# Kernel optimization log

Hardware: AMD Instinct MI355X
Metric: run time of the kernel (lower is better)

## Reference

```python
import jax, jax.numpy as jnp
import numpy as np

HIDDEN = 2048
N_LAYERS = 2
CHOICE_NUM = 19  # (task_num-1)*2 + 1 with task_num=10, adapt=False
VOCAB = CHOICE_NUM + 1


def setup_inputs() -> dict:
    key = jax.random.key(0)
    ks = jax.random.split(key, 16)
    s = 0.02
    inp = {}
    inp["input_idx"] = jax.random.randint(ks[0], (1,), 0, VOCAB)
    inp["task"] = 5  # python int; 1+task <= CHOICE_NUM
    inp["embedding"] = jax.random.normal(ks[1], (VOCAB, HIDDEN), dtype=jnp.float32) * s
    k = 2
    for i in range(N_LAYERS):
        inp[f"w_ih_{i}"] = jax.random.normal(ks[k + 0], (4 * HIDDEN, HIDDEN), dtype=jnp.float32) * s
        inp[f"w_hh_{i}"] = jax.random.normal(ks[k + 1], (4 * HIDDEN, HIDDEN), dtype=jnp.float32) * s
        inp[f"b_ih_{i}"] = jax.random.normal(ks[k + 2], (4 * HIDDEN,), dtype=jnp.float32) * s
        inp[f"b_hh_{i}"] = jax.random.normal(ks[k + 3], (4 * HIDDEN,), dtype=jnp.float32) * s
        k += 4
    inp["w_choice"] = jax.random.normal(ks[k], (CHOICE_NUM, HIDDEN), dtype=jnp.float32) * s
    inp["b_choice"] = jax.random.normal(ks[k + 1], (CHOICE_NUM,), dtype=jnp.float32) * s
    return inp


def _lstm_cell(x, h, c, w_ih, w_hh, b_ih, b_hh):
    # x, h, c: [1, H]; torch LSTMCell gate order: i, f, g, o
    gates = x @ w_ih.T + b_ih + h @ w_hh.T + b_hh  # [1, 4H]
    i, f, g, o = jnp.split(gates, 4, axis=-1)
    c_next = jax.nn.sigmoid(f) * c + jax.nn.sigmoid(i) * jnp.tanh(g)
    h_next = jax.nn.sigmoid(o) * jnp.tanh(c_next)
    return h_next, c_next


def reference(input_idx, task, embedding,
              w_ih_0, w_hh_0, b_ih_0, b_hh_0,
              w_ih_1, w_hh_1, b_ih_1, b_hh_1,
              w_choice, b_choice):
    x = embedding[input_idx].reshape(1, -1)  # [1, H]
    layers = [(w_ih_0, w_hh_0, b_ih_0, b_hh_0),
              (w_ih_1, w_hh_1, b_ih_1, b_hh_1)]
    zeros = jnp.zeros((1, HIDDEN), dtype=x.dtype)
    for (w_ih, w_hh, b_ih, b_hh) in layers:
        # hidden=None in the torch module -> per-layer zero initial state
        h, c = _lstm_cell(x, zeros, zeros, w_ih, w_hh, b_ih, b_hh)
        x = h
    logit = (x @ w_choice.T + b_choice).reshape(-1)  # [CHOICE_NUM]
    mask = jnp.arange(CHOICE_NUM) < (1 + task)  # adapt=False: prefix 1+task ones
    logit = jnp.where(mask, logit, jnp.float32(-1e9))
    return logit
```

## Files before the change

kernel.cpp:

```cpp
#include <hip/hip_runtime.h>

#define H 2048
#define CH 19

typedef float f32x4 __attribute__((ext_vector_type(4)));

__device__ __forceinline__ float wred(float s) {
    #pragma unroll
    for (int off = 32; off; off >>= 1) s += __shfl_down(s, off, 64);
    return s;
}

__device__ __forceinline__ float sigm(float v) { return 1.f / (1.f + expf(-v)); }

__device__ __forceinline__ float dot_row_nt(const float* __restrict__ rowp,
                                            const float* __restrict__ xp, int lane) {
    const f32x4* row = (const f32x4*)rowp;
    const f32x4* x   = (const f32x4*)xp;
    f32x4 w[8], v[8];
    #pragma unroll
    for (int j = 0; j < 8; ++j) w[j] = __builtin_nontemporal_load(&row[lane + j * 64]);
    #pragma unroll
    for (int j = 0; j < 8; ++j) v[j] = x[lane + j * 64];
    float s = 0.f;
    #pragma unroll
    for (int j = 0; j < 8; ++j)
        s += w[j].x * v[j].x + w[j].y * v[j].y + w[j].z * v[j].z + w[j].w * v[j].w;
    return s;
}

__global__ __launch_bounds__(192, 6) void lstm_layer_kernel(
    const float* __restrict__ w_ih, const float* __restrict__ b_ih,
    const float* __restrict__ b_hh,
    const float* __restrict__ x_base, const int* __restrict__ idx_ptr,
    float* __restrict__ h_out)
{
    const int unit = blockIdx.x;
    const int wave = threadIdx.x >> 6;
    const int lane = threadIdx.x & 63;
    const int row  = (wave == 0) ? unit : (wave == 1 ? 2 * H + unit : 3 * H + unit);

    const float* x = x_base + (idx_ptr ? (size_t)idx_ptr[0] * H : 0);
    const float bsum = b_ih[row] + b_hh[row];

    float sum = wred(dot_row_nt(w_ih + (size_t)row * H, x, lane));

    __shared__ float g[3];
    if (lane == 0) g[wave] = sum + bsum;
    __syncthreads();
    if (threadIdx.x == 0) {
        float si = sigm(g[0]);
        float so = sigm(g[2]);
        h_out[unit] = so * tanhf(si * tanhf(g[1]));
    }
}

__global__ __launch_bounds__(64) void logits_kernel(
    const float* __restrict__ wc, const float* __restrict__ bc,
    const float* __restrict__ h, const int* __restrict__ taskp,
    float* __restrict__ out)
{
    const int r = blockIdx.x;
    const int lane = threadIdx.x;
    const int task = taskp[0];
    float s = wred(dot_row_nt(wc + (size_t)r * H, h, lane));
    if (lane == 0)
        out[r] = (r < 1 + task) ? (s + bc[r]) : -1e9f;
}

extern "C" void kernel_launch(void* const* d_in, const int* in_sizes, int n_in,
                              void* d_out, int out_size, void* d_ws, size_t ws_size,
                              hipStream_t stream) {
    const int*   idx  = (const int*)d_in[0];
    const int*   task = (const int*)d_in[1];
    const float* emb  = (const float*)d_in[2];
    const float* w0   = (const float*)d_in[3];
    const float* bi0  = (const float*)d_in[5];
    const float* bh0  = (const float*)d_in[6];
    const float* w1   = (const float*)d_in[7];
    const float* bi1  = (const float*)d_in[9];
    const float* bh1  = (const float*)d_in[10];
    const float* wc   = (const float*)d_in[11];
    const float* bc   = (const float*)d_in[12];
    float* out = (float*)d_out;
    float* ws  = (float*)d_ws;

    float* h0 = ws;
    float* h1 = ws + H;

    lstm_layer_kernel<<<H, 192, 0, stream>>>(w0, bi0, bh0, emb, idx, h0);
    lstm_layer_kernel<<<H, 192, 0, stream>>>(w1, bi1, bh1, h0, nullptr, h1);
    logits_kernel<<<CH, 64, 0, stream>>>(wc, bc, h1, task, out);
}
```

Baseline: 25.38 us.

## Fuse layer-1 LSTM and logits into one kernel via sentinel flag polling

Merges the second LSTM layer and the logits projection into a single launch. The extra tail blocks preload their classifier row and spin on per-unit h1 slots until those slots are no longer the sentinel value that layer 0 writes into them. This removes one kernel launch and its inter-kernel gap, at the cost of spin-waiting blocks that occupy CUs. It also depends on the producer blocks being scheduled before or alongside the consumers, otherwise it can deadlock.

```diff
diff --git a/kernel.cpp b/kernel.cpp
--- a/kernel.cpp
+++ b/kernel.cpp
@@ -2,6 +2,7 @@
 
 #define H 2048
 #define CH 19
+#define SENT 0xFFFFFFFFu
 
 typedef float f32x4 __attribute__((ext_vector_type(4)));
 
@@ -29,20 +30,21 @@
     return s;
 }
 
-__global__ __launch_bounds__(192, 6) void lstm_layer_kernel(
+__global__ __launch_bounds__(192, 6) void layer0_kernel(
     const float* __restrict__ w_ih, const float* __restrict__ b_ih,
     const float* __restrict__ b_hh,
-    const float* __restrict__ x_base, const int* __restrict__ idx_ptr,
-    float* __restrict__ h_out)
+    const float* __restrict__ emb, const int* __restrict__ idxp,
+    float* __restrict__ h_out, unsigned* __restrict__ h1_slots)
 {
     const int unit = blockIdx.x;
+    if (threadIdx.x == 0) h1_slots[unit] = SENT;
+
     const int wave = threadIdx.x >> 6;
     const int lane = threadIdx.x & 63;
     const int row  = (wave == 0) ? unit : (wave == 1 ? 2 * H + unit : 3 * H + unit);
 
-    const float* x = x_base + (idx_ptr ? (size_t)idx_ptr[0] * H : 0);
+    const float* x = emb + (size_t)idxp[0] * H;
     const float bsum = b_ih[row] + b_hh[row];
-
     float sum = wred(dot_row_nt(w_ih + (size_t)row * H, x, lane));
 
     __shared__ float g[3];
@@ -55,17 +57,71 @@
     }
 }
 
-__global__ __launch_bounds__(64) void logits_kernel(
+__global__ __launch_bounds__(192, 6) void layer1_logits_kernel(
+    const float* __restrict__ w_ih, const float* __restrict__ b_ih,
+    const float* __restrict__ b_hh,
+    const float* __restrict__ h_in,
     const float* __restrict__ wc, const float* __restrict__ bc,
-    const float* __restrict__ h, const int* __restrict__ taskp,
-    float* __restrict__ out)
+    const int* __restrict__ taskp,
+    unsigned* __restrict__ h1_slots, float* __restrict__ out)
 {
-    const int r = blockIdx.x;
-    const int lane = threadIdx.x;
-    const int task = taskp[0];
-    float s = wred(dot_row_nt(wc + (size_t)r * H, h, lane));
-    if (lane == 0)
-        out[r] = (r < 1 + task) ? (s + bc[r]) : -1e9f;
+    if (blockIdx.x < H) {
+        const int unit = blockIdx.x;
+        const int wave = threadIdx.x >> 6;
+        const int lane = threadIdx.x & 63;
+        const int row  = (wave == 0) ? unit : (wave == 1 ? 2 * H + unit : 3 * H + unit);
+
+        const float bsum = b_ih[row] + b_hh[row];
+        float sum = wred(dot_row_nt(w_ih + (size_t)row * H, h_in, lane));
+
+        __shared__ float g[3];
+        if (lane == 0) g[wave] = sum + bsum;
+        __syncthreads();
+        if (threadIdx.x == 0) {
+            float si = sigm(g[0]);
+            float so = sigm(g[2]);
+            float h1 = so * tanhf(si * tanhf(g[1]));
+            __hip_atomic_store(&h1_slots[unit], __float_as_uint(h1),
+                               __ATOMIC_RELAXED, __HIP_MEMORY_SCOPE_AGENT);
+        }
+    } else {
+        const int r = blockIdx.x - H;
+        const int t = threadIdx.x;
+        const int task = taskp[0];
+        const float* wrow = wc + (size_t)r * H;
+
+        float wcr[11];
+        #pragma unroll
+        for (int k = 0; k < 11; ++k) {
+            int u = t + k * 192;
+            wcr[k] = (u < H) ? wrow[u] : 0.f;
+        }
+
+        float s = 0.f;
+        #pragma unroll
+        for (int k = 0; k < 11; ++k) {
+            int u = t + k * 192;
+            if (u < H) {
+                unsigned v;
+                for (;;) {
+                    v = __hip_atomic_load(&h1_slots[u], __ATOMIC_RELAXED,
+                                          __HIP_MEMORY_SCOPE_AGENT);
+                    if (v != SENT) break;
+                    __builtin_amdgcn_s_sleep(1);
+                }
+                s += wcr[k] * __uint_as_float(v);
+            }
+        }
+        s = wred(s);
+
+        __shared__ float p[3];
+        if ((t & 63) == 0) p[t >> 6] = s;
+        __syncthreads();
+        if (t == 0) {
+            float v = p[0] + p[1] + p[2] + bc[r];
+            out[r] = (r < 1 + task) ? v : -1e9f;
+        }
+    }
 }
 
 extern "C" void kernel_launch(void* const* d_in, const int* in_sizes, int n_in,
@@ -85,10 +141,10 @@
     float* out = (float*)d_out;
     float* ws  = (float*)d_ws;
 
-    float* h0 = ws;
-    float* h1 = ws + H;
+    float*    h0       = ws;
+    unsigned* h1_slots = (unsigned*)(ws + H);
 
-    lstm_layer_kernel<<<H, 192, 0, stream>>>(w0, bi0, bh0, emb, idx, h0);
-    lstm_layer_kernel<<<H, 192, 0, stream>>>(w1, bi1, bh1, h0, nullptr, h1);
-    logits_kernel<<<CH, 64, 0, stream>>>(wc, bc, h1, task, out);
+    layer0_kernel<<<H, 192, 0, stream>>>(w0, bi0, bh0, emb, idx, h0, h1_slots);
+    layer1_logits_kernel<<<H + CH, 192, 0, stream>>>(w1, bi1, bh1, h0, wc, bc, task,
+                                                     h1_slots, out);
 }
```

After: 25.12 us. No clear change (-1.0%).

## Fuse both LSTM layers and logits into one cooperative kernel with sentinel polling

Applied to the files above, without the earlier changes.

Replaces three kernel launches with a single cooperative launch in which each wave computes one hidden unit for layer 0, publishes it with an atomic store, then polls sentinel-initialized workspace to consume h0 for layer 1. Extra blocks poll h1 to compute the logits. The intent is to remove inter-kernel launch gaps and to prefetch layer-1 weights while waiting on layer-0 results. In exchange it adds a memset, host-side occupancy queries on every call, and spin-wait polling that relies on all blocks being co-resident.

```diff
diff --git a/kernel.cpp b/kernel.cpp
--- a/kernel.cpp
+++ b/kernel.cpp
@@ -1,7 +1,9 @@
 #include <hip/hip_runtime.h>
 
-#define H 2048
+#define H  2048
 #define CH 19
+#define NB 512
+#define SENT 0xFFFFFFFFu
 
 typedef float f32x4 __attribute__((ext_vector_type(4)));
 
@@ -13,23 +15,127 @@
 
 __device__ __forceinline__ float sigm(float v) { return 1.f / (1.f + expf(-v)); }
 
+__device__ __forceinline__ float dot_nt_x(const float* __restrict__ rowp,
+                                          const f32x4* __restrict__ xr, int lane) {
+    const f32x4* row = (const f32x4*)rowp;
+    f32x4 w[8];
+    #pragma unroll
+    for (int j = 0; j < 8; ++j) w[j] = __builtin_nontemporal_load(&row[lane + j * 64]);
+    float s = 0.f;
+    #pragma unroll
+    for (int j = 0; j < 8; ++j)
+        s += w[j].x * xr[j].x + w[j].y * xr[j].y + w[j].z * xr[j].z + w[j].w * xr[j].w;
+    return s;
+}
+
+__device__ __forceinline__ f32x4 poll4(const unsigned* __restrict__ p) {
+    unsigned a, b, c, d;
+    for (;;) {
+        a = __hip_atomic_load(p + 0, __ATOMIC_RELAXED, __HIP_MEMORY_SCOPE_AGENT);
+        b = __hip_atomic_load(p + 1, __ATOMIC_RELAXED, __HIP_MEMORY_SCOPE_AGENT);
+        c = __hip_atomic_load(p + 2, __ATOMIC_RELAXED, __HIP_MEMORY_SCOPE_AGENT);
+        d = __hip_atomic_load(p + 3, __ATOMIC_RELAXED, __HIP_MEMORY_SCOPE_AGENT);
+        if (a != SENT && b != SENT && c != SENT && d != SENT) break;
+        __builtin_amdgcn_s_sleep(1);
+    }
+    f32x4 r;
+    r.x = __uint_as_float(a); r.y = __uint_as_float(b);
+    r.z = __uint_as_float(c); r.w = __uint_as_float(d);
+    return r;
+}
+
+__global__ __launch_bounds__(256) void fused_all(
+    const int* __restrict__ idxp, const int* __restrict__ taskp,
+    const float* __restrict__ emb,
+    const float* __restrict__ w0, const float* __restrict__ bi0, const float* __restrict__ bh0,
+    const float* __restrict__ w1, const float* __restrict__ bi1, const float* __restrict__ bh1,
+    const float* __restrict__ wc, const float* __restrict__ bc,
+    unsigned* __restrict__ h0q, unsigned* __restrict__ h1q,
+    float* __restrict__ out)
+{
+    const int tid  = threadIdx.x;
+    const int wv   = tid >> 6;
+    const int lane = tid & 63;
+
+    if (blockIdx.x < NB) {
+        const int u = 4 * blockIdx.x + wv;
+
+        const f32x4* x4 = (const f32x4*)(emb + (size_t)idxp[0] * H);
+        f32x4 xr[8];
+        #pragma unroll
+        for (int j = 0; j < 8; ++j) xr[j] = x4[lane + j * 64];
+
+        float ai = dot_nt_x(w0 + (size_t)u * H,           xr, lane);
+        float ag = dot_nt_x(w0 + (size_t)(2 * H + u) * H, xr, lane);
+        float ao = dot_nt_x(w0 + (size_t)(3 * H + u) * H, xr, lane);
+        ai = wred(ai); ag = wred(ag); ao = wred(ao);
+        if (lane == 0) {
+            float gi = ai + bi0[u]         + bh0[u];
+            float gg = ag + bi0[2 * H + u] + bh0[2 * H + u];
+            float go = ao + bi0[3 * H + u] + bh0[3 * H + u];
+            float h0 = sigm(go) * tanhf(sigm(gi) * tanhf(gg));
+            __hip_atomic_store(&h0q[u], __float_as_uint(h0),
+                               __ATOMIC_RELAXED, __HIP_MEMORY_SCOPE_AGENT);
+        }
+
+        const f32x4* r1 = (const f32x4*)(w1 + (size_t)u * H);
+        f32x4 wb[8];
+        #pragma unroll
+        for (int j = 0; j < 8; ++j) wb[j] = __builtin_nontemporal_load(&r1[lane + j * 64]);
+
+        f32x4 hr[8];
+        #pragma unroll
+        for (int j = 0; j < 8; ++j) hr[j] = poll4(&h0q[4 * (lane + j * 64)]);
+
+        float bi_ = 0.f;
+        #pragma unroll
+        for (int j = 0; j < 8; ++j)
+            bi_ += wb[j].x * hr[j].x + wb[j].y * hr[j].y + wb[j].z * hr[j].z + wb[j].w * hr[j].w;
+        float bg_ = dot_nt_x(w1 + (size_t)(2 * H + u) * H, hr, lane);
+        float bo_ = dot_nt_x(w1 + (size_t)(3 * H + u) * H, hr, lane);
+        bi_ = wred(bi_); bg_ = wred(bg_); bo_ = wred(bo_);
+        if (lane == 0) {
+            float gi = bi_ + bi1[u]         + bh1[u];
+            float gg = bg_ + bi1[2 * H + u] + bh1[2 * H + u];
+            float go = bo_ + bi1[3 * H + u] + bh1[3 * H + u];
+            float h1 = sigm(go) * tanhf(sigm(gi) * tanhf(gg));
+            __hip_atomic_store(&h1q[u], __float_as_uint(h1),
+                               __ATOMIC_RELAXED, __HIP_MEMORY_SCOPE_AGENT);
+        }
+    } else {
+        const int r = blockIdx.x - NB;
+        const int task = taskp[0];
+        const f32x4* wr = (const f32x4*)(wc + (size_t)r * H);
+        f32x4 wa = wr[tid];
+        f32x4 wbv = wr[tid + 256];
+
+        f32x4 ha = poll4(&h1q[4 * tid]);
+        f32x4 hb = poll4(&h1q[4 * (tid + 256)]);
+
+        float s = wa.x * ha.x + wa.y * ha.y + wa.z * ha.z + wa.w * ha.w
+                + wbv.x * hb.x + wbv.y * hb.y + wbv.z * hb.z + wbv.w * hb.w;
+        s = wred(s);
+
+        __shared__ float p[4];
+        if (lane == 0) p[wv] = s;
+        __syncthreads();
+        if (tid == 0) {
+            float v = p[0] + p[1] + p[2] + p[3] + bc[r];
+            out[r] = (r < 1 + task) ? v : -1e9f;
+        }
+    }
+}
+
 __device__ __forceinline__ float dot_row_nt(const float* __restrict__ rowp,
                                             const float* __restrict__ xp, int lane) {
-    const f32x4* row = (const f32x4*)rowp;
-    const f32x4* x   = (const f32x4*)xp;
-    f32x4 w[8], v[8];
-    #pragma unroll
-    for (int j = 0; j < 8; ++j) w[j] = __builtin_nontemporal_load(&row[lane + j * 64]);
-    #pragma unroll
-    for (int j = 0; j < 8; ++j) v[j] = x[lane + j * 64];
-    float s = 0.f;
-    #pragma unroll
-    for (int j = 0; j < 8; ++j)
-        s += w[j].x * v[j].x + w[j].y * v[j].y + w[j].z * v[j].z + w[j].w * v[j].w;
-    return s;
-}
-
-__global__ __launch_bounds__(192, 6) void lstm_layer_kernel(
+    const f32x4* x = (const f32x4*)xp;
+    f32x4 xr[8];
+    #pragma unroll
+    for (int j = 0; j < 8; ++j) xr[j] = x[lane + j * 64];
+    return dot_nt_x(rowp, xr, lane);
+}
+
+__global__ __launch_bounds__(192) void lstm_layer_kernel(
     const float* __restrict__ w_ih, const float* __restrict__ b_ih,
     const float* __restrict__ b_hh,
     const float* __restrict__ x_base, const int* __restrict__ idx_ptr,
@@ -39,12 +145,9 @@
     const int wave = threadIdx.x >> 6;
     const int lane = threadIdx.x & 63;
     const int row  = (wave == 0) ? unit : (wave == 1 ? 2 * H + unit : 3 * H + unit);
-
     const float* x = x_base + (idx_ptr ? (size_t)idx_ptr[0] * H : 0);
     const float bsum = b_ih[row] + b_hh[row];
-
     float sum = wred(dot_row_nt(w_ih + (size_t)row * H, x, lane));
-
     __shared__ float g[3];
     if (lane == 0) g[wave] = sum + bsum;
     __syncthreads();
@@ -83,11 +186,31 @@
     const float* wc   = (const float*)d_in[11];
     const float* bc   = (const float*)d_in[12];
     float* out = (float*)d_out;
-    float* ws  = (float*)d_ws;
-
-    float* h0 = ws;
-    float* h1 = ws + H;
-
+
+    unsigned* h0q = (unsigned*)d_ws;
+    unsigned* h1q = h0q + H;
+
+    int dev = 0;
+    (void)hipGetDevice(&dev);
+    int numCU = 0;
+    (void)hipDeviceGetAttribute(&numCU, hipDeviceAttributeMultiprocessorCount, dev);
+    int occ = 0;
+    hipError_t oe = hipOccupancyMaxActiveBlocksPerMultiprocessor(&occ, fused_all, 256, 0);
+
+    if (oe == hipSuccess && numCU > 0 && occ * numCU >= NB + CH) {
+        hipMemsetAsync(h0q, 0xFF, 2 * H * sizeof(unsigned), stream);
+        void* args[] = {(void*)&idx, (void*)&task, (void*)&emb,
+                        (void*)&w0, (void*)&bi0, (void*)&bh0,
+                        (void*)&w1, (void*)&bi1, (void*)&bh1,
+                        (void*)&wc, (void*)&bc,
+                        (void*)&h0q, (void*)&h1q, (void*)&out};
+        hipError_t le = hipLaunchCooperativeKernel(fused_all, dim3(NB + CH),
+                                                   dim3(256), args, 0, stream);
+        if (le == hipSuccess) return;
+    }
+
+    float* h0 = (float*)d_ws;
+    float* h1 = h0 + H;
     lstm_layer_kernel<<<H, 192, 0, stream>>>(w0, bi0, bh0, emb, idx, h0);
     lstm_layer_kernel<<<H, 192, 0, stream>>>(w1, bi1, bh1, h0, nullptr, h1);
     logits_kernel<<<CH, 64, 0, stream>>>(wc, bc, h1, task, out);
```

After: 25.05 us. No clear change (-1.3%).
